# Optimization experiments

Measured on AMD Instinct MI355X. Metric: run time of the kernel, lower is better.

Reference implementation:

```python
import jax, jax.numpy as jnp
import numpy as np

N_SRC, M, K, H = 100000, 20000, 32, 128
NEG_SLOPE = 0.01  # torch LeakyReLU default


def setup_inputs() -> dict:
    key = jax.random.key(0)
    ks = jax.random.split(key, 8)
    nei = jax.random.randint(ks[0], (M, K), 0, N_SRC)
    h = jax.random.normal(ks[1], (N_SRC, 1), dtype=jnp.float32)
    h_refer = jax.random.normal(ks[2], (M, 1), dtype=jnp.float32)
    # map_l / map_r: Linear(1, H), weight init U[0,1), bias U[0,0.01)
    map_l_w = jax.random.uniform(ks[3], (H, 1), dtype=jnp.float32)
    map_l_b = jax.random.uniform(ks[4], (H,), dtype=jnp.float32) * 0.01
    map_r_w = jax.random.uniform(ks[5], (H, 1), dtype=jnp.float32)
    map_r_b = jax.random.uniform(ks[6], (H,), dtype=jnp.float32) * 0.01
    # att_inter: xavier_normal gain=1.414 on shape (1, 2H)
    std = 1.414 * np.sqrt(2.0 / (1 + 2 * H))
    att_inter = jax.random.normal(ks[7], (1, 2 * H), dtype=jnp.float32) * std
    return {"nei": nei, "h": h, "h_refer": h_refer,
            "map_l_w": map_l_w, "map_l_b": map_l_b,
            "map_r_w": map_r_w, "map_r_b": map_r_b,
            "att_inter": att_inter}


def reference(nei, h, h_refer, map_l_w, map_l_b, map_r_w, map_r_b, att_inter):
    # project scalar features to H dims
    h = jax.nn.relu(h @ map_l_w.T + map_l_b)            # [N, H]
    hr = jax.nn.relu(h_refer @ map_r_w.T + map_r_b)     # [M, H]
    nei_emb = h[nei]                                    # [M, K, H] gather
    # split attention vector to avoid materializing concat([hr, nei_emb])
    a_ref = att_inter[0, :H]                            # [H]
    a_nei = att_inter[0, H:]                            # [H]
    logits = (hr @ a_ref)[:, None] + nei_emb @ a_nei    # [M, K]
    logits = jnp.where(logits >= 0, logits, NEG_SLOPE * logits)  # leakyrelu
    att = jax.nn.softmax(logits, axis=1)                # softmax over neighbors
    lr_inner = jnp.einsum('mkh,mh->mk', nei_emb, hr)    # [M, K]
    out = jax.nn.relu(jnp.sum(att * lr_inner, axis=1, keepdims=True))  # [M, 1]
    return (out, att)
```

## Files before the change

### kernel.cpp

```cpp
#include <hip/hip_runtime.h>

#define N_SRC 100000
#define M_NODES 20000
#define K_NEI 32
#define H_DIM 128
#define NEG_SLOPE 0.01f

#define WS_T    0
#define WS_WL   128
#define WS_BL   256
#define WS_WR   384
#define WS_BR   512
#define WS_AR   640
#define WS_SA   768

__global__ __launch_bounds__(128) void prep_kernel(
    const float* __restrict__ map_l_w,
    const float* __restrict__ map_l_b,
    const float* __restrict__ map_r_w,
    const float* __restrict__ map_r_b,
    const float* __restrict__ att_inter,
    float* __restrict__ ws)
{
    __shared__ float s_t[H_DIM];
    __shared__ int   s_ord[H_DIM];
    __shared__ float s_cw[H_DIM];
    __shared__ float s_cb[H_DIM];

    const int j = threadIdx.x;
    const float wl = map_l_w[j];
    const float bl = map_l_b[j];
    const float t  = -bl / fmaxf(wl, 1e-30f);
    s_t[j] = t;
    __syncthreads();

    int rank = 0;
    #pragma unroll 8
    for (int i = 0; i < H_DIM; ++i) {
        const float ti = s_t[i];
        rank += (ti < t || (ti == t && i < j)) ? 1 : 0;
    }
    s_ord[rank] = j;
    __syncthreads();

    const int src = s_ord[j];
    const float wls = map_l_w[src];
    const float bls = map_l_b[src];
    ws[WS_T  + j] = s_t[src];
    ws[WS_WL + j] = wls;
    ws[WS_BL + j] = bls;
    ws[WS_WR + j] = map_r_w[src];
    ws[WS_BR + j] = map_r_b[src];
    ws[WS_AR + j] = att_inter[src];
    const float an = att_inter[H_DIM + src];
    s_cw[j] = an * wls;
    s_cb[j] = an * bls;
    __syncthreads();

    if (j < 8) {
        const int sb = j * 16;
        float cw[16], cb[16];
        float sw = 0.f, sbv = 0.f;
        #pragma unroll
        for (int i = 0; i < 16; ++i) {
            cw[i] = s_cw[sb + i]; cb[i] = s_cb[sb + i];
            sw += cw[i]; sbv += cb[i];
        }
        float iw = sw, ib = sbv, v;
        v = __shfl_up(iw, 1); if (j >= 1) iw += v;
        v = __shfl_up(ib, 1); if (j >= 1) ib += v;
        v = __shfl_up(iw, 2); if (j >= 2) iw += v;
        v = __shfl_up(ib, 2); if (j >= 2) ib += v;
        v = __shfl_up(iw, 4); if (j >= 4) iw += v;
        v = __shfl_up(ib, 4); if (j >= 4) ib += v;
        float rw = iw - sw, rb = ib - sbv;
        float2* sa = (float2*)(ws + WS_SA);
        #pragma unroll
        for (int i = 0; i < 16; ++i) {
            sa[sb + i] = make_float2(rw, rb);
            rw += cw[i]; rb += cb[i];
        }
        if (j == 7) sa[H_DIM] = make_float2(rw, rb);
    }
}

#define BLK_M2 16
#define SH_STRIDE 132

__global__ __launch_bounds__(128) void main_kernel(
    const int*   __restrict__ nei,
    const float* __restrict__ h,
    const float* __restrict__ h_refer,
    const float* __restrict__ ws,
    float*       __restrict__ out,
    float*       __restrict__ att)
{
    __shared__ float  s_T[H_DIM];
    __shared__ float2 s_SA[H_DIM + 1];
    __shared__ float2 s_SH[BLK_M2][SH_STRIDE];

    const int tid  = threadIdx.x;
    const int slot = tid >> 3;
    const int u    = tid & 7;
    const int m    = blockIdx.x * BLK_M2 + slot;

    const int4  nv = *(const int4*)(nei + m * K_NEI + u * 4);
    const float rm = h_refer[m];

    if (tid < H_DIM) {
        s_T[tid]  = ws[WS_T + tid];
        s_SA[tid] = ((const float2*)(ws + WS_SA))[tid];
    }
    if (tid == 0) s_SA[H_DIM] = ((const float2*)(ws + WS_SA))[H_DIM];

    const float x0 = h[nv.x], x1 = h[nv.y], x2 = h[nv.z], x3 = h[nv.w];

    const int sb = u * 16;
    float hrdot = 0.f;
    float cw[16], cb[16];
    float sw = 0.f, sbv = 0.f;
    #pragma unroll
    for (int q = 0; q < 4; ++q) {
        const float4 wr4 = *(const float4*)(ws + WS_WR + sb + q * 4);
        const float4 br4 = *(const float4*)(ws + WS_BR + sb + q * 4);
        const float4 ar4 = *(const float4*)(ws + WS_AR + sb + q * 4);
        const float4 wl4 = *(const float4*)(ws + WS_WL + sb + q * 4);
        const float4 bl4 = *(const float4*)(ws + WS_BL + sb + q * 4);
        const float h0 = fmaxf(0.f, fmaf(rm, wr4.x, br4.x));
        const float h1 = fmaxf(0.f, fmaf(rm, wr4.y, br4.y));
        const float h2 = fmaxf(0.f, fmaf(rm, wr4.z, br4.z));
        const float h3 = fmaxf(0.f, fmaf(rm, wr4.w, br4.w));
        hrdot += h0*ar4.x + h1*ar4.y + h2*ar4.z + h3*ar4.w;
        cw[q*4+0] = h0*wl4.x; cb[q*4+0] = h0*bl4.x;
        cw[q*4+1] = h1*wl4.y; cb[q*4+1] = h1*bl4.y;
        cw[q*4+2] = h2*wl4.z; cb[q*4+2] = h2*bl4.z;
        cw[q*4+3] = h3*wl4.w; cb[q*4+3] = h3*bl4.w;
        sw  += cw[q*4+0] + cw[q*4+1] + cw[q*4+2] + cw[q*4+3];
        sbv += cb[q*4+0] + cb[q*4+1] + cb[q*4+2] + cb[q*4+3];
    }
    {
        float iw = sw, ib = sbv, v;
        v = __shfl_up(iw, 1); if (u >= 1) iw += v;
        v = __shfl_up(ib, 1); if (u >= 1) ib += v;
        v = __shfl_up(iw, 2); if (u >= 2) iw += v;
        v = __shfl_up(ib, 2); if (u >= 2) ib += v;
        v = __shfl_up(iw, 4); if (u >= 4) iw += v;
        v = __shfl_up(ib, 4); if (u >= 4) ib += v;
        float rw = iw - sw, rb = ib - sbv;
        #pragma unroll
        for (int q = 0; q < 8; ++q) {
            float4 t4;
            t4.x = rw; t4.y = rb; rw += cw[q*2];   rb += cb[q*2];
            t4.z = rw; t4.w = rb; rw += cw[q*2+1]; rb += cb[q*2+1];
            *(float4*)(&s_SH[slot][sb + q*2]) = t4;
        }
        if (u == 7) s_SH[slot][H_DIM] = make_float2(rw, rb);
    }
    hrdot += __shfl_xor(hrdot, 1);
    hrdot += __shfl_xor(hrdot, 2);
    hrdot += __shfl_xor(hrdot, 4);

    __syncthreads();

    const float xs[4] = {x0, x1, x2, x3};
    float lg[4], in_[4];
    float mx = -3.4e38f;
    #pragma unroll
    for (int t = 0; t < 4; ++t) {
        const float x = xs[t];
        int r = (s_T[63] < x) ? 64 : 0;
        if (s_T[r+31] < x) r += 32;
        if (s_T[r+15] < x) r += 16;
        if (s_T[r+7]  < x) r += 8;
        if (s_T[r+3]  < x) r += 4;
        if (s_T[r+1]  < x) r += 2;
        if (s_T[r]    < x) r += 1;
        if (s_T[r]    < x) r += 1;
        const float2 sa = s_SA[r];
        const float2 sh = s_SH[slot][r];
        const float l = fmaf(sa.x, x, sa.y) + hrdot;
        lg[t]  = (l >= 0.f) ? l : NEG_SLOPE * l;
        in_[t] = fmaf(sh.x, x, sh.y);
        mx = fmaxf(mx, lg[t]);
    }
    mx = fmaxf(mx, __shfl_xor(mx, 1));
    mx = fmaxf(mx, __shfl_xor(mx, 2));
    mx = fmaxf(mx, __shfl_xor(mx, 4));

    float e[4];
    float se = 0.f, sei = 0.f;
    #pragma unroll
    for (int t = 0; t < 4; ++t) {
        e[t] = __expf(lg[t] - mx);
        se  += e[t];
        sei += e[t] * in_[t];
    }
    se  += __shfl_xor(se, 1);  se  += __shfl_xor(se, 2);  se  += __shfl_xor(se, 4);
    sei += __shfl_xor(sei, 1); sei += __shfl_xor(sei, 2); sei += __shfl_xor(sei, 4);

    const float inv = 1.0f / se;
    const float4 a4 = make_float4(e[0]*inv, e[1]*inv, e[2]*inv, e[3]*inv);
    *(float4*)(att + m * K_NEI + u * 4) = a4;
    if (u == 0) out[m] = fmaxf(0.f, sei * inv);
}

extern "C" void kernel_launch(void* const* d_in, const int* in_sizes, int n_in,
                              void* d_out, int out_size, void* d_ws, size_t ws_size,
                              hipStream_t stream) {
    const int*   nei       = (const int*)  d_in[0];
    const float* h         = (const float*)d_in[1];
    const float* h_refer   = (const float*)d_in[2];
    const float* map_l_w   = (const float*)d_in[3];
    const float* map_l_b   = (const float*)d_in[4];
    const float* map_r_w   = (const float*)d_in[5];
    const float* map_r_b   = (const float*)d_in[6];
    const float* att_inter = (const float*)d_in[7];

    float* out = (float*)d_out;
    float* att = out + M_NODES;
    float* ws  = (float*)d_ws;

    prep_kernel<<<1, 128, 0, stream>>>(
        map_l_w, map_l_b, map_r_w, map_r_b, att_inter, ws);

    const int blocks = M_NODES / BLK_M2;
    main_kernel<<<blocks, 128, 0, stream>>>(
        nei, h, h_refer, ws, out, att);
}
```

Measured before the change: 18.28 us.

## Fuse prep kernel into main kernel, recomputing threshold sort per block

Drops the single-block prep kernel and its global workspace round trip. Every main block now computes the breakpoint thresholds, ranks them with an O(H) loop per thread, permutes the weights into shared memory, and builds the prefix sums itself. This removes one kernel launch and the serial dependency between the two kernels. In exchange, each of the 1250 blocks repeats the rank sort and prefix work and uses more shared memory.

```diff
diff --git a/kernel.cpp b/kernel.cpp
--- a/kernel.cpp
+++ b/kernel.cpp
@@ -6,59 +6,72 @@
 #define H_DIM 128
 #define NEG_SLOPE 0.01f
 
-#define WS_T    0
-#define WS_WL   128
-#define WS_BL   256
-#define WS_WR   384
-#define WS_BR   512
-#define WS_AR   640
-#define WS_SA   768
-
-__global__ __launch_bounds__(128) void prep_kernel(
+#define BLK_M 16
+#define SH_STRIDE 132
+
+__global__ __launch_bounds__(128) void intra_att_fused(
+    const int*   __restrict__ nei,
+    const float* __restrict__ h,
+    const float* __restrict__ h_refer,
     const float* __restrict__ map_l_w,
     const float* __restrict__ map_l_b,
     const float* __restrict__ map_r_w,
     const float* __restrict__ map_r_b,
     const float* __restrict__ att_inter,
-    float* __restrict__ ws)
+    float*       __restrict__ out,
+    float*       __restrict__ att)
 {
-    __shared__ float s_t[H_DIM];
-    __shared__ int   s_ord[H_DIM];
-    __shared__ float s_cw[H_DIM];
-    __shared__ float s_cb[H_DIM];
-
-    const int j = threadIdx.x;
-    const float wl = map_l_w[j];
-    const float bl = map_l_b[j];
-    const float t  = -bl / fmaxf(wl, 1e-30f);
-    s_t[j] = t;
+    __shared__ float  s_traw[H_DIM];
+    __shared__ int    s_ord[H_DIM];
+    __shared__ float  s_T[H_DIM];
+    __shared__ float  s_wr[H_DIM], s_br[H_DIM], s_ar[H_DIM];
+    __shared__ float  s_wl[H_DIM], s_bl[H_DIM];
+    __shared__ float  s_cw[H_DIM], s_cb[H_DIM];
+    __shared__ float2 s_SA[H_DIM + 1];
+    __shared__ float2 s_SH[BLK_M][SH_STRIDE];
+
+    const int tid  = threadIdx.x;
+    const int slot = tid >> 3;
+    const int u    = tid & 7;
+    const int m    = blockIdx.x * BLK_M + slot;
+
+    const int4  nv = *(const int4*)(nei + m * K_NEI + u * 4);
+    const float rm = h_refer[m];
+
+    const float wl0 = map_l_w[tid];
+    const float bl0 = map_l_b[tid];
+    const float t0  = -bl0 / fmaxf(wl0, 1e-30f);
+    s_traw[tid] = t0;
     __syncthreads();
 
     int rank = 0;
     #pragma unroll 8
     for (int i = 0; i < H_DIM; ++i) {
-        const float ti = s_t[i];
-        rank += (ti < t || (ti == t && i < j)) ? 1 : 0;
-    }
-    s_ord[rank] = j;
-    __syncthreads();
-
-    const int src = s_ord[j];
+        const float ti = s_traw[i];
+        rank += (ti < t0 || (ti == t0 && i < tid)) ? 1 : 0;
+    }
+    s_ord[rank] = tid;
+
+    const float x0 = h[nv.x], x1 = h[nv.y], x2 = h[nv.z], x3 = h[nv.w];
+
+    __syncthreads();
+
+    const int   src = s_ord[tid];
     const float wls = map_l_w[src];
     const float bls = map_l_b[src];
-    ws[WS_T  + j] = s_t[src];
-    ws[WS_WL + j] = wls;
-    ws[WS_BL + j] = bls;
-    ws[WS_WR + j] = map_r_w[src];
-    ws[WS_BR + j] = map_r_b[src];
-    ws[WS_AR + j] = att_inter[src];
-    const float an = att_inter[H_DIM + src];
-    s_cw[j] = an * wls;
-    s_cb[j] = an * bls;
-    __syncthreads();
-
-    if (j < 8) {
-        const int sb = j * 16;
+    const float an  = att_inter[H_DIM + src];
+    s_T[tid]  = s_traw[src];
+    s_wl[tid] = wls;
+    s_bl[tid] = bls;
+    s_wr[tid] = map_r_w[src];
+    s_br[tid] = map_r_b[src];
+    s_ar[tid] = att_inter[src];
+    s_cw[tid] = an * wls;
+    s_cb[tid] = an * bls;
+    __syncthreads();
+
+    if (tid < 8) {
+        const int sb = tid * 16;
         float cw[16], cb[16];
         float sw = 0.f, sbv = 0.f;
         #pragma unroll
@@ -67,53 +80,20 @@
             sw += cw[i]; sbv += cb[i];
         }
         float iw = sw, ib = sbv, v;
-        v = __shfl_up(iw, 1); if (j >= 1) iw += v;
-        v = __shfl_up(ib, 1); if (j >= 1) ib += v;
-        v = __shfl_up(iw, 2); if (j >= 2) iw += v;
-        v = __shfl_up(ib, 2); if (j >= 2) ib += v;
-        v = __shfl_up(iw, 4); if (j >= 4) iw += v;
-        v = __shfl_up(ib, 4); if (j >= 4) ib += v;
+        v = __shfl_up(iw, 1); if (tid >= 1) iw += v;
+        v = __shfl_up(ib, 1); if (tid >= 1) ib += v;
+        v = __shfl_up(iw, 2); if (tid >= 2) iw += v;
+        v = __shfl_up(ib, 2); if (tid >= 2) ib += v;
+        v = __shfl_up(iw, 4); if (tid >= 4) iw += v;
+        v = __shfl_up(ib, 4); if (tid >= 4) ib += v;
         float rw = iw - sw, rb = ib - sbv;
-        float2* sa = (float2*)(ws + WS_SA);
         #pragma unroll
         for (int i = 0; i < 16; ++i) {
-            sa[sb + i] = make_float2(rw, rb);
+            s_SA[sb + i] = make_float2(rw, rb);
             rw += cw[i]; rb += cb[i];
         }
-        if (j == 7) sa[H_DIM] = make_float2(rw, rb);
-    }
-}
-
-#define BLK_M2 16
-#define SH_STRIDE 132
-
-__global__ __launch_bounds__(128) void main_kernel(
-    const int*   __restrict__ nei,
-    const float* __restrict__ h,
-    const float* __restrict__ h_refer,
-    const float* __restrict__ ws,
-    float*       __restrict__ out,
-    float*       __restrict__ att)
-{
-    __shared__ float  s_T[H_DIM];
-    __shared__ float2 s_SA[H_DIM + 1];
-    __shared__ float2 s_SH[BLK_M2][SH_STRIDE];
-
-    const int tid  = threadIdx.x;
-    const int slot = tid >> 3;
-    const int u    = tid & 7;
-    const int m    = blockIdx.x * BLK_M2 + slot;
-
-    const int4  nv = *(const int4*)(nei + m * K_NEI + u * 4);
-    const float rm = h_refer[m];
-
-    if (tid < H_DIM) {
-        s_T[tid]  = ws[WS_T + tid];
-        s_SA[tid] = ((const float2*)(ws + WS_SA))[tid];
-    }
-    if (tid == 0) s_SA[H_DIM] = ((const float2*)(ws + WS_SA))[H_DIM];
-
-    const float x0 = h[nv.x], x1 = h[nv.y], x2 = h[nv.z], x3 = h[nv.w];
+        if (tid == 7) s_SA[H_DIM] = make_float2(rw, rb);
+    }
 
     const int sb = u * 16;
     float hrdot = 0.f;
@@ -121,11 +101,11 @@
     float sw = 0.f, sbv = 0.f;
     #pragma unroll
     for (int q = 0; q < 4; ++q) {
-        const float4 wr4 = *(const float4*)(ws + WS_WR + sb + q * 4);
-        const float4 br4 = *(const float4*)(ws + WS_BR + sb + q * 4);
-        const float4 ar4 = *(const float4*)(ws + WS_AR + sb + q * 4);
-        const float4 wl4 = *(const float4*)(ws + WS_WL + sb + q * 4);
-        const float4 bl4 = *(const float4*)(ws + WS_BL + sb + q * 4);
+        const float4 wr4 = *(const float4*)(s_wr + sb + q * 4);
+        const float4 br4 = *(const float4*)(s_br + sb + q * 4);
+        const float4 ar4 = *(const float4*)(s_ar + sb + q * 4);
+        const float4 wl4 = *(const float4*)(s_wl + sb + q * 4);
+        const float4 bl4 = *(const float4*)(s_bl + sb + q * 4);
         const float h0 = fmaxf(0.f, fmaf(rm, wr4.x, br4.x));
         const float h1 = fmaxf(0.f, fmaf(rm, wr4.y, br4.y));
         const float h2 = fmaxf(0.f, fmaf(rm, wr4.z, br4.z));
@@ -218,12 +198,9 @@
 
     float* out = (float*)d_out;
     float* att = out + M_NODES;
-    float* ws  = (float*)d_ws;
-
-    prep_kernel<<<1, 128, 0, stream>>>(
-        map_l_w, map_l_b, map_r_w, map_r_b, att_inter, ws);
-
-    const int blocks = M_NODES / BLK_M2;
-    main_kernel<<<blocks, 128, 0, stream>>>(
-        nei, h, h_refer, ws, out, att);
+
+    const int blocks = M_NODES / BLK_M;
+    intra_att_fused<<<blocks, 128, 0, stream>>>(
+        nei, h, h_refer, map_l_w, map_l_b, map_r_w, map_r_b, att_inter,
+        out, att);
 }
```

Result: faster. 16.79 us (median of 2 runs) (-8.1%).
